# Kernel optimization log

Hardware: AMD Instinct MI355X
Metric: run time of the kernel (lower is better)

Reference implementation:

```python
import jax, jax.numpy as jnp
import numpy as np
import math

B, NQ, NK = 8, 1024, 2048
DQ = DK = DV = 1024
H = 8
DH = DV // H
EPS = 1e-5


def _layernorm(x, g, b):
    mu = jnp.mean(x, axis=-1, keepdims=True)
    var = jnp.mean(jnp.square(x - mu), axis=-1, keepdims=True)
    return (x - mu) * jax.lax.rsqrt(var + EPS) * g + b


def setup_inputs() -> dict:
    key = jax.random.key(0)
    ks = jax.random.split(key, 12)
    s_q = 1.0 / math.sqrt(DQ)
    s_v = 1.0 / math.sqrt(DV)
    return {
        "Q": jax.random.normal(ks[0], (B, NQ, DQ), jnp.float32),
        "K": jax.random.normal(ks[1], (B, NK, DK), jnp.float32),
        "Wq": jax.random.normal(ks[2], (DQ, DV), jnp.float32) * s_q,
        "bq": jnp.zeros((DV,), jnp.float32),
        "Wk": jax.random.normal(ks[3], (DK, DV), jnp.float32) * s_q,
        "bk": jnp.zeros((DV,), jnp.float32),
        "Wv": jax.random.normal(ks[4], (DK, DV), jnp.float32) * s_q,
        "bv": jnp.zeros((DV,), jnp.float32),
        "Wo": jax.random.normal(ks[5], (DV, DV), jnp.float32) * s_v,
        "bo": jnp.zeros((DV,), jnp.float32),
        "g0": jnp.ones((DV,), jnp.float32),
        "b0": jnp.zeros((DV,), jnp.float32),
        "g1": jnp.ones((DV,), jnp.float32),
        "b1": jnp.zeros((DV,), jnp.float32),
    }


def reference(Q, K, Wq, bq, Wk, bk, Wv, bv, Wo, bo, g0, b0, g1, b1):
    # projections
    q = Q @ Wq + bq                      # [B, NQ, DV]
    k = K @ Wk + bk                      # [B, NK, DV]
    v = K @ Wv + bv                      # [B, NK, DV]
    qh = q.reshape(B, NQ, H, DH)
    kh = k.reshape(B, NK, H, DH)
    vh = v.reshape(B, NK, H, DH)
    # NOTE: original scales by sqrt(dim_V), not sqrt(d_head)
    scale = 1.0 / math.sqrt(DV)
    logits = jnp.einsum("bqhd,bkhd->bhqk", qh, kh) * scale
    A = jax.nn.softmax(logits, axis=-1)
    # residual baked into attention output: Q_ + A @ V_
    Oh = qh + jnp.einsum("bhqk,bkhd->bqhd", A, vh)
    O = Oh.reshape(B, NQ, DV)
    O = _layernorm(O, g0, b0)
    O = O + jax.nn.relu(O @ Wo + bo)
    O = _layernorm(O, g1, b1)
    return O
```

## Files before the change

kernel.cpp:

```cpp
#include <hip/hip_runtime.h>
#include <stdint.h>

#define DEVI static __device__ __forceinline__

typedef __attribute__((ext_vector_type(8))) short short8;
typedef __attribute__((ext_vector_type(4))) float floatx4;
typedef __attribute__((ext_vector_type(4))) unsigned short ushortx4;

DEVI unsigned short f2bf(float f) {
  union { float f; uint32_t u; } v; v.f = f;
  uint32_t r = v.u + 0x7FFFu + ((v.u >> 16) & 1u);
  return (unsigned short)(r >> 16);
}
DEVI unsigned short f2bf_trunc(float f) {
  union { float f; uint32_t u; } v; v.f = f;
  return (unsigned short)(v.u >> 16);
}
DEVI float bf2f(unsigned short s) {
  union { uint32_t u; float f; } v; v.u = ((uint32_t)s) << 16;
  return v.f;
}
DEVI uint32_t fbits(float f) {
  union { float f; uint32_t u; } v; v.f = f;
  return v.u;
}
DEVI unsigned char f2fp8(float f) {
  return (unsigned char)(__builtin_amdgcn_cvt_pk_fp8_f32(f, f, 0, false) & 0xff);
}

DEVI void lds_cp16(void* lds, const void* g) {
  __builtin_amdgcn_global_load_lds(
      (const __attribute__((address_space(1))) uint32_t*)g,
      reinterpret_cast<__attribute__((address_space(3))) uint32_t*>(
          (uint32_t)reinterpret_cast<uintptr_t>(lds)),
      16, 0, 0);
}

__global__ __launch_bounds__(256) void cvt_qk(const float* __restrict__ Q,
                                              const float* __restrict__ K,
                                              unsigned short* __restrict__ Qb,
                                              unsigned char* __restrict__ Kf8) {
  const int bid = blockIdx.x;
  if (bid < 8192) {
    const size_t i = (size_t)bid * 256 + threadIdx.x;
    const floatx4 v = ((const floatx4*)Q)[i];
    ushortx4 o;
    o.x = f2bf(v.x); o.y = f2bf(v.y); o.z = f2bf(v.z); o.w = f2bf(v.w);
    ((ushortx4*)Qb)[i] = o;
  } else {
    const size_t i = (size_t)(bid - 8192) * 256 + threadIdx.x;
    const floatx4 v = ((const floatx4*)K)[i];
    int p = __builtin_amdgcn_cvt_pk_fp8_f32(v.x, v.y, 0, false);
    p = __builtin_amdgcn_cvt_pk_fp8_f32(v.z, v.w, p, true);
    ((int*)Kf8)[i] = p;
  }
}

__global__ __launch_bounds__(256) void wtrans4(const float* __restrict__ Wq,
                                               const float* __restrict__ Wk,
                                               const float* __restrict__ Wv,
                                               const float* __restrict__ Wo,
                                               unsigned short* __restrict__ Wt,
                                               unsigned char* __restrict__ Wt8) {
  __shared__ float t[32][33];
  const int tx = threadIdx.x, ty = threadIdx.y;
  const int z = blockIdx.z;
  const float* W = (z == 0) ? Wq : (z == 1) ? Wk : (z == 2) ? Wv : Wo;
  const int c0 = blockIdx.x * 32, r0 = blockIdx.y * 32;
#pragma unroll
  for (int i = 0; i < 4; i++)
    t[ty + i * 8][tx] = W[(size_t)(r0 + ty + i * 8) * 1024 + c0 + tx];
  __syncthreads();
  if (z == 0 || z == 3) {
    unsigned short* D = Wt + (z == 0 ? 0 : (size_t)1024 * 1024);
#pragma unroll
    for (int i = 0; i < 4; i++)
      D[(size_t)(c0 + ty + i * 8) * 1024 + r0 + tx] = f2bf(t[tx][ty + i * 8]);
  } else {
    unsigned char* D = Wt8 + (z == 1 ? 0 : (size_t)1024 * 1024);
#pragma unroll
    for (int i = 0; i < 4; i++)
      D[(size_t)(c0 + ty + i * 8) * 1024 + r0 + tx] = f2fp8(t[tx][ty + i * 8]);
  }
}

template <int EPI>
__global__ __launch_bounds__(256, 3) void gemm_bt(
    const unsigned short* __restrict__ A, const unsigned short* __restrict__ Bt,
    const float* __restrict__ bias, const unsigned short* __restrict__ X1,
    void* __restrict__ Cout) {
  __shared__ unsigned short As[2][4][128][8];
  __shared__ unsigned short Bs[2][4][128][8];

  const int tid = threadIdx.x;
  const int lane = tid & 63, w = tid >> 6;
  const int wr = w >> 1, wc = w & 1;
  const int qd = lane >> 4, l16 = lane & 15;
  const int bid = blockIdx.x;
  const int xcd = bid & 7, loc = bid >> 3;
  const int m0 = (xcd * 8 + (loc & 7)) * 128;
  const int n0 = (loc >> 3) * 128;

  floatx4 acc[4][4];
#pragma unroll
  for (int i = 0; i < 4; i++)
#pragma unroll
    for (int j = 0; j < 4; j++) { floatx4 z = {0.f, 0.f, 0.f, 0.f}; acc[i][j] = z; }

  const int prow = tid & 127;
  const unsigned short* aptr = A + (size_t)(m0 + prow) * 1024 + ((tid >> 7) << 3);
  const unsigned short* bptr = Bt + (size_t)(n0 + prow) * 1024 + ((tid >> 7) << 3);
  const int dstoff = tid * 8;

  lds_cp16(&As[0][0][0][0] + dstoff, aptr);
  lds_cp16(&As[0][0][0][0] + dstoff + 2048, aptr + 16);
  lds_cp16(&Bs[0][0][0][0] + dstoff, bptr);
  lds_cp16(&Bs[0][0][0][0] + dstoff + 2048, bptr + 16);

  for (int it = 0; it < 32; it++) {
    __syncthreads();
    if (it < 31) {
      const int nb = (it + 1) & 1, k0 = (it + 1) * 32;
      lds_cp16(&As[nb][0][0][0] + dstoff, aptr + k0);
      lds_cp16(&As[nb][0][0][0] + dstoff + 2048, aptr + k0 + 16);
      lds_cp16(&Bs[nb][0][0][0] + dstoff, bptr + k0);
      lds_cp16(&Bs[nb][0][0][0] + dstoff + 2048, bptr + k0 + 16);
    }
    const int cur = it & 1;
    short8 af[4], bf[4];
#pragma unroll
    for (int mi = 0; mi < 4; mi++)
      af[mi] = *(const short8*)&As[cur][qd][wr * 64 + mi * 16 + l16][0];
#pragma unroll
    for (int ni = 0; ni < 4; ni++)
      bf[ni] = *(const short8*)&Bs[cur][qd][wc * 64 + ni * 16 + l16][0];
#pragma unroll
    for (int mi = 0; mi < 4; mi++)
#pragma unroll
      for (int ni = 0; ni < 4; ni++)
        acc[mi][ni] =
            __builtin_amdgcn_mfma_f32_16x16x32_bf16(af[mi], bf[ni], acc[mi][ni], 0, 0, 0);
  }

#pragma unroll
  for (int mi = 0; mi < 4; mi++) {
#pragma unroll
    for (int ni = 0; ni < 4; ni++) {
      const int row = m0 + wr * 64 + mi * 16 + qd * 4;
      const int col = n0 + wc * 64 + ni * 16 + l16;
      const float bv = bias[col];
      if constexpr (EPI == 0) {
        unsigned short* C = (unsigned short*)Cout;
#pragma unroll
        for (int r = 0; r < 4; r++)
          C[(size_t)(row + r) * 1024 + col] = f2bf(acc[mi][ni][r] + bv);
      } else {
        float* C = (float*)Cout;
#pragma unroll
        for (int r = 0; r < 4; r++) {
          const float x1 = bf2f(X1[(size_t)(row + r) * 1024 + col]);
          C[(size_t)(row + r) * 1024 + col] = x1 + fmaxf(acc[mi][ni][r] + bv, 0.f);
        }
      }
    }
  }
}

__global__ __launch_bounds__(256, 3) void gemm_kv_f8(
    const unsigned char* __restrict__ A, const unsigned char* __restrict__ Bt,
    const float* __restrict__ biasK, const float* __restrict__ biasV,
    unsigned short* __restrict__ CK, unsigned short* __restrict__ CV) {
  __shared__ unsigned char As[2][4][128][16];
  __shared__ unsigned char Bs[2][4][128][16];

  const int tid = threadIdx.x;
  const int lane = tid & 63, w = tid >> 6;
  const int wr = w >> 1, wc = w & 1;
  const int qd = lane >> 4, l16 = lane & 15;
  const int bid = blockIdx.x;
  const int xcd = bid & 7, loc = bid >> 3;
  const int m0 = (xcd * 16 + (loc & 15)) * 128;
  const int n0 = (loc >> 4) * 128;

  floatx4 acc[4][4];
#pragma unroll
  for (int i = 0; i < 4; i++)
#pragma unroll
    for (int j = 0; j < 4; j++) { floatx4 z = {0.f, 0.f, 0.f, 0.f}; acc[i][j] = z; }

  const int srow = tid & 127, sc = tid >> 7;
  const unsigned char* aptr = A + (size_t)(m0 + srow) * 1024 + sc * 16;
  const unsigned char* bptr = Bt + (size_t)(n0 + srow) * 1024 + sc * 16;
  unsigned char* dA = &As[0][sc][srow][0];
  unsigned char* dB = &Bs[0][sc][srow][0];

  lds_cp16(dA, aptr);
  lds_cp16(dA + 4096, aptr + 32);
  lds_cp16(dB, bptr);
  lds_cp16(dB + 4096, bptr + 32);

  for (int it = 0; it < 16; it++) {
    __syncthreads();
    if (it < 15) {
      const int nb = (it + 1) & 1, k0 = (it + 1) * 64;
      lds_cp16(dA + nb * 8192, aptr + k0);
      lds_cp16(dA + nb * 8192 + 4096, aptr + k0 + 32);
      lds_cp16(dB + nb * 8192, bptr + k0);
      lds_cp16(dB + nb * 8192 + 4096, bptr + k0 + 32);
    }
    const int cur = it & 1;
    const int coff = (qd & 1) * 8, chi = qd >> 1;
    long a8[4][2], b8[4][2];
#pragma unroll
    for (int mi = 0; mi < 4; mi++) {
      const int row = wr * 64 + mi * 16 + l16;
      a8[mi][0] = *(const long*)&As[cur][chi][row][coff];
      a8[mi][1] = *(const long*)&As[cur][2 + chi][row][coff];
    }
#pragma unroll
    for (int ni = 0; ni < 4; ni++) {
      const int row = wc * 64 + ni * 16 + l16;
      b8[ni][0] = *(const long*)&Bs[cur][chi][row][coff];
      b8[ni][1] = *(const long*)&Bs[cur][2 + chi][row][coff];
    }
#pragma unroll
    for (int mi = 0; mi < 4; mi++)
#pragma unroll
      for (int ni = 0; ni < 4; ni++)
        acc[mi][ni] = __builtin_amdgcn_mfma_f32_16x16x32_fp8_fp8(
            a8[mi][0], b8[ni][0], acc[mi][ni], 0, 0, 0);
#pragma unroll
    for (int mi = 0; mi < 4; mi++)
#pragma unroll
      for (int ni = 0; ni < 4; ni++)
        acc[mi][ni] = __builtin_amdgcn_mfma_f32_16x16x32_fp8_fp8(
            a8[mi][1], b8[ni][1], acc[mi][ni], 0, 0, 0);
  }

#pragma unroll
  for (int mi = 0; mi < 4; mi++) {
#pragma unroll
    for (int ni = 0; ni < 4; ni++) {
      const int row = m0 + wr * 64 + mi * 16 + qd * 4;
      const int col = n0 + wc * 64 + ni * 16 + l16;
      if (col < 1024) {
        const float bv = biasK[col];
#pragma unroll
        for (int r = 0; r < 4; r++)
          CK[(size_t)(row + r) * 1024 + col] = f2bf(acc[mi][ni][r] + bv);
      } else {
        const int vc = col - 1024;
        const float bv = biasV[vc];
        const int bb = row >> 11, nk = row & 2047;
        const int hh = vc >> 7, dh = vc & 127;
        ushortx4 pk;
        pk.x = f2bf(acc[mi][ni][0] + bv);
        pk.y = f2bf(acc[mi][ni][1] + bv);
        pk.z = f2bf(acc[mi][ni][2] + bv);
        pk.w = f2bf(acc[mi][ni][3] + bv);
        *(ushortx4*)&CV[(size_t)((bb * 8 + hh) * 128 + dh) * 2048 + nk] = pk;
      }
    }
  }
}

__global__ __launch_bounds__(256, 3) void attn(
    const unsigned short* __restrict__ qb, const unsigned short* __restrict__ kb,
    const unsigned short* __restrict__ vt, unsigned short* __restrict__ Ob) {
  __shared__ unsigned short smem[16384];

  const int tid = threadIdx.x;
  const int lane = tid & 63, w = tid >> 6;
  const int qd = lane >> 4, l16 = lane & 15;
  const int bid = blockIdx.x;
  const int qt = bid >> 6, bh = bid & 63;
  const int h = bh >> 3, b = bh & 7;
  const int m0 = qt * 128;

  const size_t qbase = ((size_t)(b * 1024 + m0)) * 1024 + h * 128;
  const size_t kbase = ((size_t)(b * 2048)) * 1024 + h * 128;
  const size_t vbase = ((size_t)((b * 8 + h) * 128)) * 2048;

#pragma unroll
  for (int i = 0; i < 8; i++) {
    const int p = i * 256 + tid;
    const int row = p & 127, c = p >> 7;
    lds_cp16(&smem[c * 1024 + row * 8], qb + qbase + (size_t)row * 1024 + c * 8);
  }
  __syncthreads();
  short8 qf[2][4];
#pragma unroll
  for (int nt = 0; nt < 2; nt++)
#pragma unroll
    for (int ks = 0; ks < 4; ks++)
      qf[nt][ks] =
          *(const short8*)&smem[(ks * 4 + qd) * 1024 + (w * 32 + nt * 16 + l16) * 8];
  __syncthreads();

#pragma unroll
  for (int i = 0; i < 2; i++) {
    const int p = i * 256 + tid;
    const int kr = p & 31, kc = p >> 5;
    lds_cp16(&smem[kc * 256 + kr * 8], kb + kbase + (size_t)kr * 1024 + kc * 8);
    const int dh = p & 127, vc = p >> 7;
    lds_cp16(&smem[8192 + vc * 1024 + dh * 8], vt + vbase + (size_t)dh * 2048 + vc * 8);
  }

  floatx4 oacc[8][2];
#pragma unroll
  for (int mt = 0; mt < 8; mt++)
#pragma unroll
    for (int nt = 0; nt < 2; nt++) { floatx4 z = {0.f, 0.f, 0.f, 0.f}; oacc[mt][nt] = z; }
  float lsum[2] = {0.f, 0.f};

  const int addrLo = ((qd & 1) * 32 + l16) * 4;
  const int addrHi = addrLo + 64;
  const bool loHalf = (lane < 32);

  for (int it = 0; it < 64; it++) {
    __syncthreads();
    if (it + 1 < 64) {
      const int nb = (it + 1) & 1, kv0 = (it + 1) * 32;
#pragma unroll
      for (int i = 0; i < 2; i++) {
        const int p = i * 256 + tid;
        const int kr = p & 31, kc = p >> 5;
        lds_cp16(&smem[nb * 4096 + kc * 256 + kr * 8],
                 kb + kbase + (size_t)(kv0 + kr) * 1024 + kc * 8);
        const int dh = p & 127, vc = p >> 7;
        lds_cp16(&smem[8192 + nb * 4096 + vc * 1024 + dh * 8],
                 vt + vbase + (size_t)dh * 2048 + kv0 + vc * 8);
      }
    }
    const int cur = it & 1;

    floatx4 st[2][2];
#pragma unroll
    for (int mt = 0; mt < 2; mt++)
#pragma unroll
      for (int nt = 0; nt < 2; nt++) { floatx4 z = {0.f, 0.f, 0.f, 0.f}; st[mt][nt] = z; }
#pragma unroll
    for (int ks = 0; ks < 4; ks++) {
      const short8 ka = *(const short8*)&smem[cur * 4096 + (ks * 4 + qd) * 256 + l16 * 8];
      const short8 kb2 =
          *(const short8*)&smem[cur * 4096 + (ks * 4 + qd) * 256 + (16 + l16) * 8];
#pragma unroll
      for (int nt = 0; nt < 2; nt++) {
        st[0][nt] = __builtin_amdgcn_mfma_f32_16x16x32_bf16(ka, qf[nt][ks], st[0][nt], 0, 0, 0);
        st[1][nt] = __builtin_amdgcn_mfma_f32_16x16x32_bf16(kb2, qf[nt][ks], st[1][nt], 0, 0, 0);
      }
    }

    uint32_t pk[2][2][2];
#pragma unroll
    for (int mt = 0; mt < 2; mt++)
#pragma unroll
      for (int nt = 0; nt < 2; nt++) {
        const float e0 = __expf(st[mt][nt][0] * 0.03125f);
        const float e1 = __expf(st[mt][nt][1] * 0.03125f);
        const float e2 = __expf(st[mt][nt][2] * 0.03125f);
        const float e3 = __expf(st[mt][nt][3] * 0.03125f);
        lsum[nt] += (e0 + e1) + (e2 + e3);
        pk[mt][nt][0] = __builtin_amdgcn_perm(fbits(e1), fbits(e0), 0x07060302);
        pk[mt][nt][1] = __builtin_amdgcn_perm(fbits(e3), fbits(e2), 0x07060302);
      }

#pragma unroll
    for (int nt = 0; nt < 2; nt++) {
      int d0a = __builtin_amdgcn_ds_bpermute(addrLo, (int)pk[0][nt][0]);
      int d0b = __builtin_amdgcn_ds_bpermute(addrLo, (int)pk[1][nt][0]);
      int d1a = __builtin_amdgcn_ds_bpermute(addrLo, (int)pk[0][nt][1]);
      int d1b = __builtin_amdgcn_ds_bpermute(addrLo, (int)pk[1][nt][1]);
      int d2a = __builtin_amdgcn_ds_bpermute(addrHi, (int)pk[0][nt][0]);
      int d2b = __builtin_amdgcn_ds_bpermute(addrHi, (int)pk[1][nt][0]);
      int d3a = __builtin_amdgcn_ds_bpermute(addrHi, (int)pk[0][nt][1]);
      int d3b = __builtin_amdgcn_ds_bpermute(addrHi, (int)pk[1][nt][1]);
      union { int i[4]; short8 s; } u;
      u.i[0] = loHalf ? d0a : d0b;
      u.i[1] = loHalf ? d1a : d1b;
      u.i[2] = loHalf ? d2a : d2b;
      u.i[3] = loHalf ? d3a : d3b;
      const short8 pf = u.s;
#pragma unroll
      for (int mt = 0; mt < 8; mt++) {
        const short8 vf =
            *(const short8*)&smem[8192 + cur * 4096 + qd * 1024 + (mt * 16 + l16) * 8];
        oacc[mt][nt] = __builtin_amdgcn_mfma_f32_16x16x32_bf16(vf, pf, oacc[mt][nt], 0, 0, 0);
      }
    }
  }

  float inv[2];
#pragma unroll
  for (int nt = 0; nt < 2; nt++) {
    float s = lsum[nt];
    s += __shfl_xor(s, 16);
    s += __shfl_xor(s, 32);
    inv[nt] = 1.f / s;
  }

  __syncthreads();
#pragma unroll
  for (int mt = 0; mt < 8; mt++)
#pragma unroll
    for (int nt = 0; nt < 2; nt++) {
      const int q = w * 32 + nt * 16 + l16;
#pragma unroll
      for (int r = 0; r < 4; r++) {
        const int dh = mt * 16 + qd * 4 + r;
        const int c = dh >> 3, off = dh & 7;
        smem[q * 128 + ((c ^ (q & 15)) * 8) + off] = f2bf_trunc(oacc[mt][nt][r] * inv[nt]);
      }
    }
  __syncthreads();
#pragma unroll
  for (int i = 0; i < 8; i++) {
    const int p = i * 256 + tid;
    const int row = p >> 4, c = p & 15;
    const short8 ov = *(const short8*)&smem[row * 128 + ((c ^ (row & 15)) * 8)];
    const short8 qres = *(const short8*)(qb + qbase + (size_t)row * 1024 + c * 8);
    union { unsigned short us[8]; short8 s; } o;
#pragma unroll
    for (int e = 0; e < 8; e++)
      o.us[e] = f2bf(bf2f((unsigned short)ov[e]) + bf2f((unsigned short)qres[e]));
    *(short8*)(Ob + qbase + (size_t)row * 1024 + c * 8) = o.s;
  }
}

__global__ __launch_bounds__(256) void ln_rows(const unsigned short* __restrict__ X,
                                               const float* __restrict__ g,
                                               const float* __restrict__ bb,
                                               unsigned short* __restrict__ Y) {
  __shared__ float red[8];
  const int row = blockIdx.x, tid = threadIdx.x;
  const int w = tid >> 6, lane = tid & 63;
  const ushortx4 u = ((const ushortx4*)(X + (size_t)row * 1024))[tid];
  float x0 = bf2f(u.x), x1 = bf2f(u.y), x2 = bf2f(u.z), x3 = bf2f(u.w);
  float s = x0 + x1 + x2 + x3;
  float s2 = x0 * x0 + x1 * x1 + x2 * x2 + x3 * x3;
#pragma unroll
  for (int off = 1; off < 64; off <<= 1) { s += __shfl_xor(s, off); s2 += __shfl_xor(s2, off); }
  if (lane == 0) { red[w] = s; red[4 + w] = s2; }
  __syncthreads();
  s = red[0] + red[1] + red[2] + red[3];
  s2 = red[4] + red[5] + red[6] + red[7];
  const float mu = s * (1.f / 1024.f);
  const float rs = rsqrtf(s2 * (1.f / 1024.f) - mu * mu + 1e-5f);
  const floatx4 gv = ((const floatx4*)g)[tid];
  const floatx4 bv = ((const floatx4*)bb)[tid];
  ushortx4 o;
  o.x = f2bf((x0 - mu) * rs * gv.x + bv.x);
  o.y = f2bf((x1 - mu) * rs * gv.y + bv.y);
  o.z = f2bf((x2 - mu) * rs * gv.z + bv.z);
  o.w = f2bf((x3 - mu) * rs * gv.w + bv.w);
  ((ushortx4*)(Y + (size_t)row * 1024))[tid] = o;
}

__global__ __launch_bounds__(256) void ln_f32(const float* __restrict__ X,
                                              const float* __restrict__ g,
                                              const float* __restrict__ bb,
                                              float* __restrict__ out) {
  __shared__ float red[8];
  const int row = blockIdx.x, tid = threadIdx.x;
  const int w = tid >> 6, lane = tid & 63;
  const floatx4 xv = ((const floatx4*)(X + (size_t)row * 1024))[tid];
  float x0 = xv.x, x1 = xv.y, x2 = xv.z, x3 = xv.w;
  float s = x0 + x1 + x2 + x3;
  float s2 = x0 * x0 + x1 * x1 + x2 * x2 + x3 * x3;
#pragma unroll
  for (int off = 1; off < 64; off <<= 1) { s += __shfl_xor(s, off); s2 += __shfl_xor(s2, off); }
  if (lane == 0) { red[w] = s; red[4 + w] = s2; }
  __syncthreads();
  s = red[0] + red[1] + red[2] + red[3];
  s2 = red[4] + red[5] + red[6] + red[7];
  const float mu = s * (1.f / 1024.f);
  const float rs = rsqrtf(s2 * (1.f / 1024.f) - mu * mu + 1e-5f);
  const floatx4 gv = ((const floatx4*)g)[tid];
  const floatx4 bv = ((const floatx4*)bb)[tid];
  floatx4 o;
  o.x = (x0 - mu) * rs * gv.x + bv.x;
  o.y = (x1 - mu) * rs * gv.y + bv.y;
  o.z = (x2 - mu) * rs * gv.z + bv.z;
  o.w = (x3 - mu) * rs * gv.w + bv.w;
  ((floatx4*)(out + (size_t)row * 1024))[tid] = o;
}

extern "C" void kernel_launch(void* const* d_in, const int* in_sizes, int n_in,
                              void* d_out, int out_size, void* d_ws, size_t ws_size,
                              hipStream_t stream) {
  (void)in_sizes; (void)n_in; (void)out_size; (void)ws_size;
  const float* Q  = (const float*)d_in[0];
  const float* K  = (const float*)d_in[1];
  const float* Wq = (const float*)d_in[2];
  const float* bq = (const float*)d_in[3];
  const float* Wk = (const float*)d_in[4];
  const float* bk = (const float*)d_in[5];
  const float* Wv = (const float*)d_in[6];
  const float* bv = (const float*)d_in[7];
  const float* Wo = (const float*)d_in[8];
  const float* bo = (const float*)d_in[9];
  const float* g0 = (const float*)d_in[10];
  const float* b0 = (const float*)d_in[11];
  const float* g1 = (const float*)d_in[12];
  const float* b1 = (const float*)d_in[13];
  float* out = (float*)d_out;

  char* ws = (char*)d_ws;
  const size_t MB = 1u << 20;
  unsigned short* Qb  = (unsigned short*)(ws + 0);
  unsigned short* X1  = (unsigned short*)(ws + 16 * MB);
  unsigned short* Wt  = (unsigned short*)(ws + 32 * MB);
  unsigned char*  Wt8 = (unsigned char*)(ws + 36 * MB);
  unsigned char*  Kf8 = (unsigned char*)(ws + 38 * MB);
  unsigned short* qbp = (unsigned short*)(ws + 54 * MB);
  unsigned short* kbp = (unsigned short*)(ws + 70 * MB);
  unsigned short* vtp = (unsigned short*)(ws + 102 * MB);
  unsigned short* O   = Qb;
  float* O2 = (float*)(ws + 70 * MB);

  unsigned short* Wqt = Wt;
  unsigned short* Wot = Wt + (size_t)1024 * 1024;

  cvt_qk<<<24576, 256, 0, stream>>>(Q, K, Qb, Kf8);
  wtrans4<<<dim3(32, 32, 4), dim3(32, 8), 0, stream>>>(Wq, Wk, Wv, Wo, Wt, Wt8);

  gemm_bt<0><<<512, 256, 0, stream>>>(Qb, Wqt, bq, nullptr, qbp);
  gemm_kv_f8<<<2048, 256, 0, stream>>>(Kf8, Wt8, bk, bv, kbp, vtp);
  attn<<<512, 256, 0, stream>>>(qbp, kbp, vtp, O);
  ln_rows<<<8192, 256, 0, stream>>>(O, g0, b0, X1);
  gemm_bt<2><<<512, 256, 0, stream>>>(X1, Wot, bo, X1, O2);
  ln_f32<<<8192, 256, 0, stream>>>(O2, g1, b1, out);
}
```

Measured before the change: 432.7 us.

## Store V and attention probabilities in FP8 and use FP8 MFMA for PV

The KV projection now writes V as packed FP8 in a blocked layout instead of transposed bf16, halving V traffic into the attention kernel and its shared-memory footprint. In attention, the unnormalised softmax probabilities are packed to FP8 and the P·V product uses the fp8×fp8 16x16x32 MFMA with 8-byte operands, which also halves the bpermute shuffles. V fragments are preloaded into registers before the exp phase, and s_setprio raises wave priority around the MFMA blocks. The cost is lower precision in the PV product and probability values, so accuracy could suffer.

```diff
diff --git a/kernel.cpp b/kernel.cpp
--- a/kernel.cpp
+++ b/kernel.cpp
@@ -169,7 +169,7 @@
 __global__ __launch_bounds__(256, 3) void gemm_kv_f8(
     const unsigned char* __restrict__ A, const unsigned char* __restrict__ Bt,
     const float* __restrict__ biasK, const float* __restrict__ biasV,
-    unsigned short* __restrict__ CK, unsigned short* __restrict__ CV) {
+    unsigned short* __restrict__ CK, unsigned char* __restrict__ CV8) {
   __shared__ unsigned char As[2][4][128][16];
   __shared__ unsigned char Bs[2][4][128][16];
 
@@ -253,12 +253,12 @@
         const float bv = biasV[vc];
         const int bb = row >> 11, nk = row & 2047;
         const int hh = vc >> 7, dh = vc & 127;
-        ushortx4 pk;
-        pk.x = f2bf(acc[mi][ni][0] + bv);
-        pk.y = f2bf(acc[mi][ni][1] + bv);
-        pk.z = f2bf(acc[mi][ni][2] + bv);
-        pk.w = f2bf(acc[mi][ni][3] + bv);
-        *(ushortx4*)&CV[(size_t)((bb * 8 + hh) * 128 + dh) * 2048 + nk] = pk;
+        int p = __builtin_amdgcn_cvt_pk_fp8_f32(acc[mi][ni][0] + bv,
+                                                acc[mi][ni][1] + bv, 0, false);
+        p = __builtin_amdgcn_cvt_pk_fp8_f32(acc[mi][ni][2] + bv,
+                                            acc[mi][ni][3] + bv, p, true);
+        *(uint32_t*)&CV8[((((size_t)(bb * 8 + hh)) * 256 + (nk >> 3)) * 128 + dh) * 8 +
+                         (nk & 7)] = (uint32_t)p;
       }
     }
   }
@@ -266,8 +266,9 @@
 
 __global__ __launch_bounds__(256, 3) void attn(
     const unsigned short* __restrict__ qb, const unsigned short* __restrict__ kb,
-    const unsigned short* __restrict__ vt, unsigned short* __restrict__ Ob) {
-  __shared__ unsigned short smem[16384];
+    const unsigned char* __restrict__ vt8, unsigned short* __restrict__ Ob) {
+  __shared__ __align__(16) unsigned char smc[32768];
+  unsigned short* sm16 = (unsigned short*)smc;
 
   const int tid = threadIdx.x;
   const int lane = tid & 63, w = tid >> 6;
@@ -279,13 +280,13 @@
 
   const size_t qbase = ((size_t)(b * 1024 + m0)) * 1024 + h * 128;
   const size_t kbase = ((size_t)(b * 2048)) * 1024 + h * 128;
-  const size_t vbase = ((size_t)((b * 8 + h) * 128)) * 2048;
+  const size_t vbase8 = (size_t)(b * 8 + h) * 262144;
 
 #pragma unroll
   for (int i = 0; i < 8; i++) {
     const int p = i * 256 + tid;
     const int row = p & 127, c = p >> 7;
-    lds_cp16(&smem[c * 1024 + row * 8], qb + qbase + (size_t)row * 1024 + c * 8);
+    lds_cp16(&sm16[c * 1024 + row * 8], qb + qbase + (size_t)row * 1024 + c * 8);
   }
   __syncthreads();
   short8 qf[2][4];
@@ -294,16 +295,18 @@
 #pragma unroll
     for (int ks = 0; ks < 4; ks++)
       qf[nt][ks] =
-          *(const short8*)&smem[(ks * 4 + qd) * 1024 + (w * 32 + nt * 16 + l16) * 8];
+          *(const short8*)&sm16[(ks * 4 + qd) * 1024 + (w * 32 + nt * 16 + l16) * 8];
   __syncthreads();
 
 #pragma unroll
   for (int i = 0; i < 2; i++) {
     const int p = i * 256 + tid;
     const int kr = p & 31, kc = p >> 5;
-    lds_cp16(&smem[kc * 256 + kr * 8], kb + kbase + (size_t)kr * 1024 + kc * 8);
-    const int dh = p & 127, vc = p >> 7;
-    lds_cp16(&smem[8192 + vc * 1024 + dh * 8], vt + vbase + (size_t)dh * 2048 + vc * 8);
+    lds_cp16(smc + kc * 512 + kr * 16, kb + kbase + (size_t)kr * 1024 + kc * 8);
+  }
+  {
+    const int vc = tid >> 6, d2 = (tid & 63) * 2;
+    lds_cp16(smc + 16384 + vc * 1024 + d2 * 8, vt8 + vbase8 + vc * 1024 + d2 * 8);
   }
 
   floatx4 oacc[8][2];
@@ -325,11 +328,13 @@
       for (int i = 0; i < 2; i++) {
         const int p = i * 256 + tid;
         const int kr = p & 31, kc = p >> 5;
-        lds_cp16(&smem[nb * 4096 + kc * 256 + kr * 8],
+        lds_cp16(smc + nb * 8192 + kc * 512 + kr * 16,
                  kb + kbase + (size_t)(kv0 + kr) * 1024 + kc * 8);
-        const int dh = p & 127, vc = p >> 7;
-        lds_cp16(&smem[8192 + nb * 4096 + vc * 1024 + dh * 8],
-                 vt + vbase + (size_t)dh * 2048 + kv0 + vc * 8);
+      }
+      {
+        const int vc = tid >> 6, d2 = (tid & 63) * 2;
+        lds_cp16(smc + 16384 + nb * 4096 + vc * 1024 + d2 * 8,
+                 vt8 + vbase8 + (size_t)kv0 * 128 + vc * 1024 + d2 * 8);
       }
     }
     const int cur = it & 1;
@@ -339,19 +344,27 @@
     for (int mt = 0; mt < 2; mt++)
 #pragma unroll
       for (int nt = 0; nt < 2; nt++) { floatx4 z = {0.f, 0.f, 0.f, 0.f}; st[mt][nt] = z; }
+    __builtin_amdgcn_s_setprio(1);
 #pragma unroll
     for (int ks = 0; ks < 4; ks++) {
-      const short8 ka = *(const short8*)&smem[cur * 4096 + (ks * 4 + qd) * 256 + l16 * 8];
+      const short8 ka =
+          *(const short8*)(smc + cur * 8192 + (ks * 4 + qd) * 512 + l16 * 16);
       const short8 kb2 =
-          *(const short8*)&smem[cur * 4096 + (ks * 4 + qd) * 256 + (16 + l16) * 8];
+          *(const short8*)(smc + cur * 8192 + (ks * 4 + qd) * 512 + (16 + l16) * 16);
 #pragma unroll
       for (int nt = 0; nt < 2; nt++) {
         st[0][nt] = __builtin_amdgcn_mfma_f32_16x16x32_bf16(ka, qf[nt][ks], st[0][nt], 0, 0, 0);
         st[1][nt] = __builtin_amdgcn_mfma_f32_16x16x32_bf16(kb2, qf[nt][ks], st[1][nt], 0, 0, 0);
       }
     }
-
-    uint32_t pk[2][2][2];
+    __builtin_amdgcn_s_setprio(0);
+
+    long vl[8];
+#pragma unroll
+    for (int mt = 0; mt < 8; mt++)
+      vl[mt] = *(const long*)(smc + 16384 + cur * 4096 + qd * 1024 + (mt * 16 + l16) * 8);
+
+    uint32_t pkf[2][2];
 #pragma unroll
     for (int mt = 0; mt < 2; mt++)
 #pragma unroll
@@ -361,32 +374,27 @@
         const float e2 = __expf(st[mt][nt][2] * 0.03125f);
         const float e3 = __expf(st[mt][nt][3] * 0.03125f);
         lsum[nt] += (e0 + e1) + (e2 + e3);
-        pk[mt][nt][0] = __builtin_amdgcn_perm(fbits(e1), fbits(e0), 0x07060302);
-        pk[mt][nt][1] = __builtin_amdgcn_perm(fbits(e3), fbits(e2), 0x07060302);
+        int p = __builtin_amdgcn_cvt_pk_fp8_f32(e0, e1, 0, false);
+        p = __builtin_amdgcn_cvt_pk_fp8_f32(e2, e3, p, true);
+        pkf[mt][nt] = (uint32_t)p;
       }
 
 #pragma unroll
     for (int nt = 0; nt < 2; nt++) {
-      int d0a = __builtin_amdgcn_ds_bpermute(addrLo, (int)pk[0][nt][0]);
-      int d0b = __builtin_amdgcn_ds_bpermute(addrLo, (int)pk[1][nt][0]);
-      int d1a = __builtin_amdgcn_ds_bpermute(addrLo, (int)pk[0][nt][1]);
-      int d1b = __builtin_amdgcn_ds_bpermute(addrLo, (int)pk[1][nt][1]);
-      int d2a = __builtin_amdgcn_ds_bpermute(addrHi, (int)pk[0][nt][0]);
-      int d2b = __builtin_amdgcn_ds_bpermute(addrHi, (int)pk[1][nt][0]);
-      int d3a = __builtin_amdgcn_ds_bpermute(addrHi, (int)pk[0][nt][1]);
-      int d3b = __builtin_amdgcn_ds_bpermute(addrHi, (int)pk[1][nt][1]);
-      union { int i[4]; short8 s; } u;
-      u.i[0] = loHalf ? d0a : d0b;
-      u.i[1] = loHalf ? d1a : d1b;
-      u.i[2] = loHalf ? d2a : d2b;
-      u.i[3] = loHalf ? d3a : d3b;
-      const short8 pf = u.s;
-#pragma unroll
-      for (int mt = 0; mt < 8; mt++) {
-        const short8 vf =
-            *(const short8*)&smem[8192 + cur * 4096 + qd * 1024 + (mt * 16 + l16) * 8];
-        oacc[mt][nt] = __builtin_amdgcn_mfma_f32_16x16x32_bf16(vf, pf, oacc[mt][nt], 0, 0, 0);
-      }
+      int lo0 = __builtin_amdgcn_ds_bpermute(addrLo, (int)pkf[0][nt]);
+      int lo1 = __builtin_amdgcn_ds_bpermute(addrLo, (int)pkf[1][nt]);
+      int hi0 = __builtin_amdgcn_ds_bpermute(addrHi, (int)pkf[0][nt]);
+      int hi1 = __builtin_amdgcn_ds_bpermute(addrHi, (int)pkf[1][nt]);
+      union { int i[2]; long l; } u;
+      u.i[0] = loHalf ? lo0 : lo1;
+      u.i[1] = loHalf ? hi0 : hi1;
+      const long pfl = u.l;
+      __builtin_amdgcn_s_setprio(1);
+#pragma unroll
+      for (int mt = 0; mt < 8; mt++)
+        oacc[mt][nt] =
+            __builtin_amdgcn_mfma_f32_16x16x32_fp8_fp8(vl[mt], pfl, oacc[mt][nt], 0, 0, 0);
+      __builtin_amdgcn_s_setprio(0);
     }
   }
 
@@ -409,7 +417,7 @@
       for (int r = 0; r < 4; r++) {
         const int dh = mt * 16 + qd * 4 + r;
         const int c = dh >> 3, off = dh & 7;
-        smem[q * 128 + ((c ^ (q & 15)) * 8) + off] = f2bf_trunc(oacc[mt][nt][r] * inv[nt]);
+        sm16[q * 128 + ((c ^ (q & 15)) * 8) + off] = f2bf_trunc(oacc[mt][nt][r] * inv[nt]);
       }
     }
   __syncthreads();
@@ -417,7 +425,7 @@
   for (int i = 0; i < 8; i++) {
     const int p = i * 256 + tid;
     const int row = p >> 4, c = p & 15;
-    const short8 ov = *(const short8*)&smem[row * 128 + ((c ^ (row & 15)) * 8)];
+    const short8 ov = *(const short8*)&sm16[row * 128 + ((c ^ (row & 15)) * 8)];
     const short8 qres = *(const short8*)(qb + qbase + (size_t)row * 1024 + c * 8);
     union { unsigned short us[8]; short8 s; } o;
 #pragma unroll
@@ -514,7 +522,7 @@
   unsigned char*  Kf8 = (unsigned char*)(ws + 38 * MB);
   unsigned short* qbp = (unsigned short*)(ws + 54 * MB);
   unsigned short* kbp = (unsigned short*)(ws + 70 * MB);
-  unsigned short* vtp = (unsigned short*)(ws + 102 * MB);
+  unsigned char*  vt8 = (unsigned char*)(ws + 102 * MB);
   unsigned short* O   = Qb;
   float* O2 = (float*)(ws + 70 * MB);
 
@@ -525,8 +533,8 @@
   wtrans4<<<dim3(32, 32, 4), dim3(32, 8), 0, stream>>>(Wq, Wk, Wv, Wo, Wt, Wt8);
 
   gemm_bt<0><<<512, 256, 0, stream>>>(Qb, Wqt, bq, nullptr, qbp);
-  gemm_kv_f8<<<2048, 256, 0, stream>>>(Kf8, Wt8, bk, bv, kbp, vtp);
-  attn<<<512, 256, 0, stream>>>(qbp, kbp, vtp, O);
+  gemm_kv_f8<<<2048, 256, 0, stream>>>(Kf8, Wt8, bk, bv, kbp, vt8);
+  attn<<<512, 256, 0, stream>>>(qbp, kbp, vt8, O);
   ln_rows<<<8192, 256, 0, stream>>>(O, g0, b0, X1);
   gemm_bt<2><<<512, 256, 0, stream>>>(X1, Wot, bo, X1, O2);
   ln_f32<<<8192, 256, 0, stream>>>(O2, g1, b1, out);
```

Measured after the change: 412.9 us. 1.05x faster.
